# Kernel tuning notes

Hardware: AMD Instinct MI355X
Metric: run time of the kernel (lower is better)

Reference implementation:

```python
import jax, jax.numpy as jnp
import numpy as np

D = 768
H = 12
DH = D // H
PAIRS4 = [(0, 1), (0, 2), (0, 3), (1, 2), (1, 3), (2, 3)]
J6 = jnp.array([[0,0,0,0,0,1],[0,0,0,0,-1,0],[0,0,0,1,0,0],[0,0,1,0,0,0],[0,-1,0,0,0,0],[1,0,0,0,0,0]], dtype=jnp.float32)


def exterior(p1, p2):
    # p1,p2: (..., 4) -> normalized Plucker coords (..., 6)
    parts = [p1[..., i] * p2[..., j] - p1[..., j] * p2[..., i] for i, j in PAIRS4]
    L = jnp.stack(parts, axis=-1)
    n = jnp.clip(jnp.linalg.norm(L, axis=-1, keepdims=True), 1e-12)
    return L / n


def layernorm(x, g, b, eps=1e-5):
    m = jnp.mean(x, axis=-1, keepdims=True)
    v = jnp.var(x, axis=-1, keepdims=True)
    return (x - m) * jax.lax.rsqrt(v + eps) * g + b


def setup_inputs() -> dict:
    key = jax.random.key(0)
    ks = jax.random.split(key, 16)
    s = 0.02
    inp = {
        'x': jax.random.normal(ks[0], (1, 2048, D), dtype=jnp.float32),
        'ln1_g': jnp.ones((D,), jnp.float32), 'ln1_b': jnp.zeros((D,), jnp.float32),
        'qkv_w': jax.random.normal(ks[1], (D, 3 * D), jnp.float32) * s,
        'qkv_b': jnp.zeros((3 * D,), jnp.float32),
        'w1_write': jax.random.normal(ks[2], (D, 4 * H), jnp.float32) * s,
        'w2_write': jax.random.normal(ks[3], (D, 4 * H), jnp.float32) * s,
        'w1_read': jax.random.normal(ks[4], (D, 4 * H), jnp.float32) * s,
        'w2_read': jax.random.normal(ks[5], (D, 4 * H), jnp.float32) * s,
        'geo_v_w': jax.random.normal(ks[6], (D, D), jnp.float32) * s,
        'geo_v_b': jnp.zeros((D,), jnp.float32),
        'gate_w': jax.random.normal(ks[7], (D, H), jnp.float32) * s,
        'gate_b': jnp.zeros((H,), jnp.float32),
        'inc_scale': jnp.ones((H,), jnp.float32),
        'out_w': jax.random.normal(ks[8], (D, D), jnp.float32) * s,
        'out_b': jnp.zeros((D,), jnp.float32),
        'ln2_g': jnp.ones((D,), jnp.float32), 'ln2_b': jnp.zeros((D,), jnp.float32),
        'fc_w': jax.random.normal(ks[9], (D, 4 * D), jnp.float32) * s,
        'fc_b': jnp.zeros((4 * D,), jnp.float32),
        'proj_w': jax.random.normal(ks[10], (4 * D, D), jnp.float32) * s,
        'proj_b': jnp.zeros((D,), jnp.float32),
    }
    return inp


def dual_path_attention(x, qkv_w, qkv_b, w1_write, w2_write, w1_read, w2_read,
                        geo_v_w, geo_v_b, gate_w, gate_b, inc_scale, out_w, out_b):
    B, T, _ = x.shape
    scale = DH ** -0.5
    qkv = (x @ qkv_w + qkv_b).reshape(B, T, 3, H, DH)
    q = qkv[:, :, 0].transpose(0, 2, 1, 3)  # (B,H,T,dh)
    k = qkv[:, :, 1].transpose(0, 2, 1, 3)
    v = qkv[:, :, 2].transpose(0, 2, 1, 3)
    std_logits = jnp.einsum('bhtd,bhsd->bhts', q, k) * scale

    x_prev = jnp.concatenate([jnp.zeros((B, 1, x.shape[-1]), x.dtype), x[:, :-1]], axis=1)
    w1 = (x_prev @ w1_write).reshape(B, T, H, 4)
    w2 = (x @ w2_write).reshape(B, T, H, 4)
    write_lines = exterior(w1, w2)  # (B,T,H,6)
    r1 = (x @ w1_read).reshape(B, T, H, 4)
    r2 = (x @ w2_read).reshape(B, T, H, 4)
    read_lines = exterior(r1, r2)
    J_write = jnp.einsum('bthi,ij->bthj', write_lines, J6)
    geo_logits = jnp.einsum('bthp,bshp->bhts', read_lines, J_write)
    geo_logits = geo_logits * inc_scale[None, :, None, None]

    mask = jnp.triu(jnp.ones((T, T), dtype=bool), k=1)  # True above diagonal
    neg = jnp.finfo(x.dtype).min
    std_attn = jax.nn.softmax(jnp.where(mask, neg, std_logits), axis=-1)
    std_out = jnp.einsum('bhts,bhsd->bthd', std_attn, v).reshape(B, T, -1)
    geo_attn = jax.nn.softmax(jnp.where(mask, neg, geo_logits), axis=-1)
    geo_v = (x @ geo_v_w + geo_v_b).reshape(B, T, H, DH).transpose(0, 2, 1, 3)
    geo_out = jnp.einsum('bhts,bhsd->bthd', geo_attn, geo_v).reshape(B, T, -1)

    gate = jax.nn.sigmoid(x @ gate_w + gate_b).mean(axis=-1, keepdims=True)
    combined = (1 - gate) * std_out + gate * geo_out
    return combined @ out_w + out_b


def reference(x, ln1_g, ln1_b, qkv_w, qkv_b, w1_write, w2_write, w1_read, w2_read,
              geo_v_w, geo_v_b, gate_w, gate_b, inc_scale, out_w, out_b,
              ln2_g, ln2_b, fc_w, fc_b, proj_w, proj_b):
    h = x + dual_path_attention(layernorm(x, ln1_g, ln1_b), qkv_w, qkv_b,
                                w1_write, w2_write, w1_read, w2_read,
                                geo_v_w, geo_v_b, gate_w, gate_b, inc_scale,
                                out_w, out_b)
    m = layernorm(h, ln2_g, ln2_b)
    mlp = jax.nn.gelu(m @ fc_w + fc_b) @ proj_w + proj_b
    return h + mlp
```

## Files before the change

### kernel.cpp

```cpp
#include <hip/hip_runtime.h>
#include <hip/hip_bf16.h>
#include <math.h>

#define TT 2048
#define DD 768

typedef __bf16 bf16x8 __attribute__((ext_vector_type(8)));
typedef float f32x4 __attribute__((ext_vector_type(4)));

__device__ __forceinline__ void gload16(const void* g, void* l) {
    __builtin_amdgcn_global_load_lds(
        (const __attribute__((address_space(1))) unsigned int*)g,
        (__attribute__((address_space(3))) unsigned int*)l, 16, 0, 0);
}

__device__ __forceinline__ bf16x8 zero8() {
    bf16x8 v;
    #pragma unroll
    for (int j = 0; j < 8; ++j) v[j] = (__bf16)0.0f;
    return v;
}

__device__ __forceinline__ const __hip_bfloat16* opart_cptr(
    const __hip_bfloat16* pA, const __hip_bfloat16* pB, const __hip_bfloat16* pC, int slot)
{
    if (slot < 192) return pA + (size_t)slot * 8192;
    if (slot < 576) return pB + (size_t)(slot - 192) * 8192;
    return pC + (size_t)(slot - 576) * 8192;
}

__global__ __launch_bounds__(256) void ln_kernel(const float* __restrict__ in,
    const float* __restrict__ g, const float* __restrict__ b,
    __hip_bfloat16* __restrict__ out)
{
    const int t = blockIdx.x;
    const int tid = threadIdx.x;
    const float* row = in + (size_t)t * DD;
    float x0 = row[tid], x1 = row[tid + 256], x2 = row[tid + 512];
    float s = x0 + x1 + x2;
    float q = x0 * x0 + x1 * x1 + x2 * x2;
    #pragma unroll
    for (int m = 1; m < 64; m <<= 1) {
        s += __shfl_xor(s, m);
        q += __shfl_xor(q, m);
    }
    __shared__ float ssum[4], sqsum[4];
    const int w = tid >> 6;
    if ((tid & 63) == 0) { ssum[w] = s; sqsum[w] = q; }
    __syncthreads();
    s = ssum[0] + ssum[1] + ssum[2] + ssum[3];
    q = sqsum[0] + sqsum[1] + sqsum[2] + sqsum[3];
    const float mean = s * (1.0f / DD);
    const float var = q * (1.0f / DD) - mean * mean;
    const float rs = rsqrtf(var + 1e-5f);
    __hip_bfloat16* orow = out + (size_t)t * DD;
    orow[tid]       = __float2bfloat16((x0 - mean) * rs * g[tid]       + b[tid]);
    orow[tid + 256] = __float2bfloat16((x1 - mean) * rs * g[tid + 256] + b[tid + 256]);
    orow[tid + 512] = __float2bfloat16((x2 - mean) * rs * g[tid + 512] + b[tid + 512]);
}

__global__ __launch_bounds__(256) void castT_kernel(const float* __restrict__ in,
    __hip_bfloat16* __restrict__ out, int K, int N)
{
    __shared__ float t[32][33];
    const int n0 = blockIdx.x << 5, k0 = blockIdx.y << 5;
    const int tx = threadIdx.x & 31, ty = threadIdx.x >> 5;
    #pragma unroll
    for (int i = 0; i < 32; i += 8)
        t[ty + i][tx] = in[(size_t)(k0 + ty + i) * N + n0 + tx];
    __syncthreads();
    #pragma unroll
    for (int i = 0; i < 32; i += 8)
        out[(size_t)(n0 + ty + i) * K + k0 + tx] = __float2bfloat16(t[tx][ty + i]);
}

__global__ __launch_bounds__(256) void wcat_kernel(
    const float* __restrict__ w2w, const float* __restrict__ w1w,
    const float* __restrict__ w1r, const float* __restrict__ w2r,
    const float* __restrict__ gw, const float* __restrict__ qkv_b,
    const float* __restrict__ gvb, __hip_bfloat16* __restrict__ Wcat,
    float* __restrict__ bias3)
{
    const int bid = blockIdx.x;
    const int tid = threadIdx.x;
    if (bid >= 204) {
        const int idx = (bid - 204) * 256 + tid;
        float v = (idx < 2304) ? qkv_b[idx] : ((idx < 3072) ? gvb[idx - 2304] : 0.f);
        bias3[idx] = v;
        return;
    }
    const float* src; int col, stride;
    if (bid < 48)       { src = w2w; col = bid;       stride = 48; }
    else if (bid < 96)  { src = w1w; col = bid - 48;  stride = 48; }
    else if (bid < 144) { src = w1r; col = bid - 96;  stride = 48; }
    else if (bid < 192) { src = w2r; col = bid - 144; stride = 48; }
    else                { src = gw;  col = bid - 192; stride = 12; }
    #pragma unroll
    for (int i = 0; i < 3; ++i) {
        const int k = tid + (i << 8);
        Wcat[(size_t)bid * 768 + k] = __float2bfloat16(src[(size_t)k * stride + col]);
    }
}

__device__ __forceinline__ float gelu_f(float x) {
    float u = 0.7978845608028654f * (x + 0.044715f * x * x * x);
    return 0.5f * x * (1.0f + tanhf(u));
}

__global__ __launch_bounds__(256) void mgemm64_kernel(
    const __hip_bfloat16* __restrict__ A, const __hip_bfloat16* __restrict__ Bt,
    const float* __restrict__ bias, const float* __restrict__ resid,
    void* __restrict__ Cout, float* __restrict__ Pb0, float* __restrict__ Pb1,
    int M, int N, int K, int kz, int epi, int omode)
{
    __shared__ __hip_bfloat16 As[64 * 32];
    __shared__ __hip_bfloat16 Bs[128 * 32];
    const int tid = threadIdx.x;
    const int lane = tid & 63, w = tid >> 6;
    const int colBase = blockIdx.x << 7, rowBase = blockIdx.y << 6;
    const int z = blockIdx.z;
    const int Kc = K / kz, koff = z * Kc;

    const int lr = lane >> 2, pc = lane & 3;
    const int n = lane & 15, quad = lane >> 4;

    const int arow = (w << 4) + lr;
    const int ac = (pc ^ ((arow >> 1) & 3)) << 3;
    const int brow0 = (w << 5) + lr, brow1 = brow0 + 16;
    const int bc0 = (pc ^ ((brow0 >> 1) & 3)) << 3;
    const int bc1 = (pc ^ ((brow1 >> 1) & 3)) << 3;

    f32x4 acc[8];
    #pragma unroll
    for (int j = 0; j < 8; ++j) acc[j] = (f32x4){0.f, 0.f, 0.f, 0.f};

    const int arF = (w << 4) + n;
    const int aposF = (quad ^ ((arF >> 1) & 3)) << 3;

    for (int kk = koff; kk < koff + Kc; kk += 32) {
        __syncthreads();
        gload16(A  + (size_t)(rowBase + arow) * K + kk + ac,   &As[(w << 4) * 32]);
        gload16(Bt + (size_t)(colBase + brow0) * K + kk + bc0, &Bs[(w << 5) * 32]);
        gload16(Bt + (size_t)(colBase + brow1) * K + kk + bc1, &Bs[((w << 5) + 16) * 32]);
        __syncthreads();

        bf16x8 af = *(const bf16x8*)&As[arF * 32 + aposF];
        #pragma unroll
        for (int j = 0; j < 8; ++j) {
            const int rb = (j << 4) + n;
            bf16x8 bfj = *(const bf16x8*)&Bs[rb * 32 + ((quad ^ ((rb >> 1) & 3)) << 3)];
            acc[j] = __builtin_amdgcn_mfma_f32_16x16x32_bf16(af, bfj, acc[j], 0, 0, 0);
        }
    }

    if (kz == 1) {
        #pragma unroll
        for (int j = 0; j < 8; ++j) {
            const int col = colBase + (j << 4) + n;
            const float bj = bias ? bias[col] : 0.f;
            #pragma unroll
            for (int r = 0; r < 4; ++r) {
                const int row = rowBase + (w << 4) + (quad << 2) + r;
                float v = acc[j][r] + bj;
                if (epi == 1) v = gelu_f(v);
                else if (epi == 2) v += resid[(size_t)row * N + col];
                if (omode == 1) ((__hip_bfloat16*)Cout)[(size_t)row * N + col] = __float2bfloat16(v);
                else ((float*)Cout)[(size_t)row * N + col] = v;
            }
        }
    } else {
        float* P = (z == 0) ? Pb0 : Pb1;
        #pragma unroll
        for (int j = 0; j < 8; ++j) {
            const int col = colBase + (j << 4) + n;
            #pragma unroll
            for (int r = 0; r < 4; ++r) {
                const int row = rowBase + (w << 4) + (quad << 2) + r;
                P[(size_t)row * N + col] = acc[j][r];
            }
        }
    }
}

__global__ __launch_bounds__(256) void kred_kernel(
    const float* __restrict__ p0, const float* __restrict__ p1,
    const float* __restrict__ bias, const float* __restrict__ resid,
    float* __restrict__ out, int N)
{
    const int base = (blockIdx.x * 256 + threadIdx.x) << 2;
    float4 a = *(const float4*)&p0[base];
    float4 b = *(const float4*)&p1[base];
    float4 bi = *(const float4*)&bias[base % N];
    float4 rs = *(const float4*)&resid[base];
    float4 o;
    o.x = a.x + b.x + bi.x + rs.x;
    o.y = a.y + b.y + bi.y + rs.y;
    o.z = a.z + b.z + bi.z + rs.z;
    o.w = a.w + b.w + bi.w + rs.w;
    *(float4*)&out[base] = o;
}

__device__ __forceinline__ void exterior6(const float* a, const float* b, float* L) {
    L[0] = a[0] * b[1] - a[1] * b[0];
    L[1] = a[0] * b[2] - a[2] * b[0];
    L[2] = a[0] * b[3] - a[3] * b[0];
    L[3] = a[1] * b[2] - a[2] * b[1];
    L[4] = a[1] * b[3] - a[3] * b[1];
    L[5] = a[2] * b[3] - a[3] * b[2];
    float n = sqrtf(L[0]*L[0] + L[1]*L[1] + L[2]*L[2] + L[3]*L[3] + L[4]*L[4] + L[5]*L[5]);
    float inv = 1.f / fmaxf(n, 1e-12f);
    #pragma unroll
    for (int p = 0; p < 6; ++p) L[p] *= inv;
}

__global__ __launch_bounds__(64) void extgate_kernel(
    const __hip_bfloat16* __restrict__ Pall, const float* __restrict__ gb,
    __hip_bfloat16* __restrict__ rlb, __hip_bfloat16* __restrict__ jwb,
    float* __restrict__ gate)
{
    const int t = blockIdx.x;
    const int tid = threadIdx.x;
    const __hip_bfloat16* row = Pall + (size_t)t * 3328 + 3072;
    if (tid < 12) {
        const int h = tid;
        float a[4], b[4], L[6];
        #pragma unroll
        for (int i = 0; i < 4; ++i) {
            a[i] = (t > 0) ? __bfloat162float(row[-3328 + 48 + h * 4 + i]) : 0.f;
            b[i] = __bfloat162float(row[h * 4 + i]);
        }
        exterior6(a, b, L);
        __hip_bfloat16* jwp = jwb + (size_t)h * 16384 + t * 8;
        jwp[0] = __float2bfloat16( L[5]); jwp[1] = __float2bfloat16(-L[4]);
        jwp[2] = __float2bfloat16( L[3]); jwp[3] = __float2bfloat16( L[2]);
        jwp[4] = __float2bfloat16(-L[1]); jwp[5] = __float2bfloat16( L[0]);
        jwp[6] = __float2bfloat16(0.f);   jwp[7] = __float2bfloat16(0.f);
        #pragma unroll
        for (int i = 0; i < 4; ++i) {
            a[i] = __bfloat162float(row[96 + h * 4 + i]);
            b[i] = __bfloat162float(row[144 + h * 4 + i]);
        }
        exterior6(a, b, L);
        __hip_bfloat16* rlp = rlb + (size_t)h * 16384 + t * 8;
        #pragma unroll
        for (int p = 0; p < 6; ++p) rlp[p] = __float2bfloat16(L[p]);
        rlp[6] = __float2bfloat16(0.f); rlp[7] = __float2bfloat16(0.f);
    }
    if (tid == 32) {
        float g = 0.f;
        #pragma unroll
        for (int i = 0; i < 12; ++i)
            g += 1.f / (1.f + __expf(-(__bfloat162float(row[192 + i]) + gb[i])));
        gate[t] = g * (1.f / 12.f);
    }
}

__global__ __launch_bounds__(256) void vt_kernel(
    const __hip_bfloat16* __restrict__ qkvAll,
    __hip_bfloat16* __restrict__ VT, __hip_bfloat16* __restrict__ GVT)
{
    __shared__ __hip_bfloat16 tile[64][72];
    const int s0 = blockIdx.x << 6, h = blockIdx.y;
    const bool isGV = (blockIdx.z != 0);
    const __hip_bfloat16* src = qkvAll + (isGV ? 2304 : 1536) + h * 64;
    __hip_bfloat16* dst = (isGV ? GVT : VT) + (size_t)h * 131072;
    const int tid = threadIdx.x;
    const int r = tid >> 2, c = (tid & 3) << 3;
    *(bf16x8*)&tile[r][c]      = *(const bf16x8*)&src[(size_t)(s0 + r) * 3328 + c];
    *(bf16x8*)&tile[r][c + 32] = *(const bf16x8*)&src[(size_t)(s0 + r) * 3328 + c + 32];
    __syncthreads();
    __hip_bfloat16 tmp[8];
    #pragma unroll
    for (int j = 0; j < 8; ++j) tmp[j] = tile[c + j][r];
    *(bf16x8*)&dst[(size_t)r * 2048 + s0 + c] = *(const bf16x8*)tmp;
    #pragma unroll
    for (int j = 0; j < 8; ++j) tmp[j] = tile[c + 32 + j][r];
    *(bf16x8*)&dst[(size_t)r * 2048 + s0 + c + 32] = *(const bf16x8*)tmp;
}

__global__ __launch_bounds__(256) void mattn_kernel(
    const __hip_bfloat16* __restrict__ qkvAll, const __hip_bfloat16* __restrict__ VT,
    const __hip_bfloat16* __restrict__ GVT, const __hip_bfloat16* __restrict__ rlb,
    const __hip_bfloat16* __restrict__ jwb, const float* __restrict__ gate,
    const float* __restrict__ inc_scale, __hip_bfloat16* __restrict__ comb,
    __hip_bfloat16* __restrict__ OpA, __hip_bfloat16* __restrict__ OpB,
    __hip_bfloat16* __restrict__ OpC, float* __restrict__ stats)
{
    __shared__ __hip_bfloat16 Ks0[2048], Ks1[2048];
    __shared__ __hip_bfloat16 VTs0[2048], VTs1[2048];
    __shared__ __hip_bfloat16 GVTs0[2048], GVTs1[2048];
    __shared__ __hip_bfloat16 JWs[64][8];
    __shared__ __bf16 Ps[64][72];

    const int j = blockIdx.x;
    const int hh = blockIdx.y;
    int qt = 0, acc = 0, nc = 1;
    #pragma unroll 1
    for (;;) {
        nc = (qt + 9) / 9;
        if (j < acc + nc) break;
        acc += nc; ++qt;
    }
    const int c = j - acc;
    const int q0 = qt << 6;
    const int nk = qt + 1;
    const int ktb = c * nk / nc;
    const int kte = (c + 1) * nk / nc - 1;
    const int tid = threadIdx.x;
    const int w = tid >> 6, lane = tid & 63;
    const int n = lane & 15, quad = lane >> 4;

    const int qrow = q0 + (w << 4) + n;
    const size_t qb = (size_t)qrow * 3328 + hh * 64;
    bf16x8 af0 = *(const bf16x8*)&qkvAll[qb + (quad << 3)];
    bf16x8 af1 = *(const bf16x8*)&qkvAll[qb + 32 + (quad << 3)];
    bf16x8 rlA = zero8();
    if (quad == 0) rlA = *(const bf16x8*)&rlb[(size_t)hh * 16384 + (size_t)qrow * 8];
    const float isc = inc_scale[hh];
    const float mgc = fabsf(isc);
    const size_t vbase = (size_t)hh * 131072;

    const int sRow = tid >> 2, sc = tid & 3;
    const int sPos = ((sc ^ ((sRow >> 1) & 3)) << 3);
    const int sOff = sc << 3;

    f32x4 Os[4], Og[4];
    float m_s[4], lsp[4], lgp[4];
    #pragma unroll
    for (int r = 0; r < 4; ++r) {
        m_s[r] = -1e30f; lsp[r] = 0.f; lgp[r] = 0.f;
        Os[r] = (f32x4){0.f, 0.f, 0.f, 0.f};
        Og[r] = (f32x4){0.f, 0.f, 0.f, 0.f};
    }

    bf16x8 rK0, rK1, rV0, rV1, rG0, rG1, rJ = zero8();
    {
        const int k0 = ktb << 6;
        const size_t kb = (size_t)(k0 + sRow) * 3328 + 768 + hh * 64;
        const size_t vb = vbase + (size_t)sRow * 2048 + k0;
        rK0 = *(const bf16x8*)&qkvAll[kb + sOff];
        rK1 = *(const bf16x8*)&qkvAll[kb + sOff + 32];
        rV0 = *(const bf16x8*)&VT[vb + sOff];
        rV1 = *(const bf16x8*)&VT[vb + sOff + 32];
        rG0 = *(const bf16x8*)&GVT[vb + sOff];
        rG1 = *(const bf16x8*)&GVT[vb + sOff + 32];
        if (tid < 64) rJ = *(const bf16x8*)&jwb[(size_t)hh * 16384 + (size_t)(k0 + tid) * 8];
    }

    for (int kt = ktb; kt <= kte; ++kt) {
        const int k0 = kt << 6;
        __syncthreads();
        *(bf16x8*)&Ks0[sRow * 32 + sPos]  = rK0;
        *(bf16x8*)&Ks1[sRow * 32 + sPos]  = rK1;
        *(bf16x8*)&VTs0[sRow * 32 + sPos] = rV0;
        *(bf16x8*)&VTs1[sRow * 32 + sPos] = rV1;
        *(bf16x8*)&GVTs0[sRow * 32 + sPos] = rG0;
        *(bf16x8*)&GVTs1[sRow * 32 + sPos] = rG1;
        if (tid < 64) *(bf16x8*)&JWs[tid][0] = rJ;
        if (kt < kte) {
            const int k1 = (kt + 1) << 6;
            const size_t kb = (size_t)(k1 + sRow) * 3328 + 768 + hh * 64;
            const size_t vb = vbase + (size_t)sRow * 2048 + k1;
            rK0 = *(const bf16x8*)&qkvAll[kb + sOff];
            rK1 = *(const bf16x8*)&qkvAll[kb + sOff + 32];
            rV0 = *(const bf16x8*)&VT[vb + sOff];
            rV1 = *(const bf16x8*)&VT[vb + sOff + 32];
            rG0 = *(const bf16x8*)&GVT[vb + sOff];
            rG1 = *(const bf16x8*)&GVT[vb + sOff + 32];
            if (tid < 64) rJ = *(const bf16x8*)&jwb[(size_t)hh * 16384 + (size_t)(k1 + tid) * 8];
        }
        __syncthreads();

        f32x4 Ss[4], Sg[4];
        #pragma unroll
        for (int t = 0; t < 4; ++t) {
            Ss[t] = (f32x4){0.f, 0.f, 0.f, 0.f};
            Sg[t] = (f32x4){0.f, 0.f, 0.f, 0.f};
        }
        #pragma unroll
        for (int t = 0; t < 4; ++t) {
            const int krow = (t << 4) + n;
            const int kpos = ((quad ^ ((krow >> 1) & 3)) << 3);
            bf16x8 kb0 = *(const bf16x8*)&Ks0[krow * 32 + kpos];
            bf16x8 kb1 = *(const bf16x8*)&Ks1[krow * 32 + kpos];
            Ss[t] = __builtin_amdgcn_mfma_f32_16x16x32_bf16(af0, kb0, Ss[t], 0, 0, 0);
            Ss[t] = __builtin_amdgcn_mfma_f32_16x16x32_bf16(af1, kb1, Ss[t], 0, 0, 0);
            bf16x8 jb = zero8();
            if (quad == 0) jb = *(const bf16x8*)&JWs[krow][0];
            Sg[t] = __builtin_amdgcn_mfma_f32_16x16x32_bf16(rlA, jb, Sg[t], 0, 0, 0);
        }
        #pragma unroll
        for (int t = 0; t < 4; ++t) {
            #pragma unroll
            for (int r = 0; r < 4; ++r) { Ss[t][r] *= 0.125f; Sg[t][r] *= isc; }
        }
        if (kt == qt) {
            #pragma unroll
            for (int t = 0; t < 4; ++t) {
                const int sg = k0 + (t << 4) + n;
                #pragma unroll
                for (int r = 0; r < 4; ++r) {
                    const int qg = q0 + (w << 4) + (quad << 2) + r;
                    if (sg > qg) { Ss[t][r] = -1e30f; Sg[t][r] = -1e30f; }
                }
            }
        }

        #pragma unroll
        for (int r = 0; r < 4; ++r) {
            float mx = fmaxf(fmaxf(Ss[0][r], Ss[1][r]), fmaxf(Ss[2][r], Ss[3][r]));
            #pragma unroll
            for (int mk = 1; mk < 16; mk <<= 1) mx = fmaxf(mx, __shfl_xor(mx, mk));
            float mnew = fmaxf(m_s[r], mx);
            float alpha = __expf(m_s[r] - mnew);
            m_s[r] = mnew;
            float sm = 0.f;
            #pragma unroll
            for (int t = 0; t < 4; ++t) { Ss[t][r] = __expf(Ss[t][r] - mnew); sm += Ss[t][r]; }
            lsp[r] = lsp[r] * alpha + sm;
            #pragma unroll
            for (int t = 0; t < 4; ++t) Os[t][r] *= alpha;

            float smg = 0.f;
            #pragma unroll
            for (int t = 0; t < 4; ++t) { Sg[t][r] = __expf(Sg[t][r] - mgc); smg += Sg[t][r]; }
            lgp[r] += smg;
        }

        #pragma unroll
        for (int t = 0; t < 4; ++t) {
            #pragma unroll
            for (int r = 0; r < 4; ++r)
                Ps[(w << 4) + (quad << 2) + r][(t << 4) + n] = (__bf16)Ss[t][r];
        }
        asm volatile("s_waitcnt lgkmcnt(0)" ::: "memory");
        #pragma unroll
        for (int st = 0; st < 2; ++st) {
            bf16x8 ap = *(const bf16x8*)&Ps[(w << 4) + n][(st << 5) + (quad << 3)];
            const __hip_bfloat16* Vh = st ? VTs1 : VTs0;
            #pragma unroll
            for (int dt = 0; dt < 4; ++dt) {
                const int vrow = (dt << 4) + n;
                const int vpos = ((quad ^ ((vrow >> 1) & 3)) << 3);
                bf16x8 vb2 = *(const bf16x8*)&Vh[vrow * 32 + vpos];
                Os[dt] = __builtin_amdgcn_mfma_f32_16x16x32_bf16(ap, vb2, Os[dt], 0, 0, 0);
            }
        }
        asm volatile("s_waitcnt lgkmcnt(0)" ::: "memory");

        #pragma unroll
        for (int t = 0; t < 4; ++t) {
            #pragma unroll
            for (int r = 0; r < 4; ++r)
                Ps[(w << 4) + (quad << 2) + r][(t << 4) + n] = (__bf16)Sg[t][r];
        }
        asm volatile("s_waitcnt lgkmcnt(0)" ::: "memory");
        #pragma unroll
        for (int st = 0; st < 2; ++st) {
            bf16x8 gp = *(const bf16x8*)&Ps[(w << 4) + n][(st << 5) + (quad << 3)];
            const __hip_bfloat16* Gh = st ? GVTs1 : GVTs0;
            #pragma unroll
            for (int dt = 0; dt < 4; ++dt) {
                const int vrow = (dt << 4) + n;
                const int vpos = ((quad ^ ((vrow >> 1) & 3)) << 3);
                bf16x8 gb2 = *(const bf16x8*)&Gh[vrow * 32 + vpos];
                Og[dt] = __builtin_amdgcn_mfma_f32_16x16x32_bf16(gp, gb2, Og[dt], 0, 0, 0);
            }
        }
    }

    float l_s[4], l_g[4];
    #pragma unroll
    for (int r = 0; r < 4; ++r) {
        float ls = lsp[r], lg = lgp[r];
        #pragma unroll
        for (int mk = 1; mk < 16; mk <<= 1) {
            ls += __shfl_xor(ls, mk);
            lg += __shfl_xor(lg, mk);
        }
        l_s[r] = ls; l_g[r] = lg;
    }

    if (nc == 1) {
        #pragma unroll
        for (int r = 0; r < 4; ++r) {
            const int row = q0 + (w << 4) + (quad << 2) + r;
            const float g = gate[row];
            const float invs = (1.f - g) / l_s[r], invg = g / l_g[r];
            #pragma unroll
            for (int dt = 0; dt < 4; ++dt) {
                float val = Os[dt][r] * invs + Og[dt][r] * invg;
                comb[(size_t)row * DD + hh * 64 + (dt << 4) + n] = __float2bfloat16(val);
            }
        }
    } else {
        const int slot = hh * 74 + acc + c;
        __hip_bfloat16* op = (__hip_bfloat16*)opart_cptr(OpA, OpB, OpC, slot);
        float* st = stats + (size_t)slot * 256;
        #pragma unroll
        for (int r = 0; r < 4; ++r) {
            const int rloc = (w << 4) + (quad << 2) + r;
            #pragma unroll
            for (int dt = 0; dt < 4; ++dt) {
                const int col = (dt << 4) + n;
                op[rloc * 128 + col]      = __float2bfloat16(Os[dt][r]);
                op[rloc * 128 + 64 + col] = __float2bfloat16(Og[dt][r]);
            }
            if (n == 0) {
                st[rloc * 4 + 0] = m_s[r]; st[rloc * 4 + 1] = l_s[r];
                st[rloc * 4 + 2] = mgc;    st[rloc * 4 + 3] = l_g[r];
            }
        }
    }
}

__global__ __launch_bounds__(256) void acomb_kernel(
    const __hip_bfloat16* __restrict__ OpA, const __hip_bfloat16* __restrict__ OpB,
    const __hip_bfloat16* __restrict__ OpC, const float* __restrict__ stats,
    const float* __restrict__ gate, __hip_bfloat16* __restrict__ comb)
{
    const int qt = 9 + blockIdx.x;
    const int h = blockIdx.y;
    const int nc = (qt + 9) / 9;
    int acc = 0;
    #pragma unroll 1
    for (int q = 0; q < qt; ++q) acc += (q + 9) / 9;
    const int sb = h * 74 + acc;
    const int tid = threadIdx.x;
    const int rloc = tid >> 2;
    const int cseg = (tid & 3) << 4;
    const int row = (qt << 6) + rloc;
    float ms = -1e30f, mg = -1e30f;
    for (int c = 0; c < nc; ++c) {
        const float* st = stats + (size_t)(sb + c) * 256 + rloc * 4;
        ms = fmaxf(ms, st[0]);
        mg = fmaxf(mg, st[2]);
    }
    float wsc[4], wgc[4];
    float ls = 0.f, lg = 0.f;
    for (int c = 0; c < nc; ++c) {
        const float* st = stats + (size_t)(sb + c) * 256 + rloc * 4;
        wsc[c] = __expf(st[0] - ms); ls += st[1] * wsc[c];
        wgc[c] = __expf(st[2] - mg); lg += st[3] * wgc[c];
    }
    const float g = gate[row];
    const float fs = (1.f - g) / ls, fg = g / lg;
    #pragma unroll
    for (int cc = 0; cc < 16; ++cc) {
        const int col = cseg + cc;
        float os = 0.f, og = 0.f;
        for (int c = 0; c < nc; ++c) {
            const __hip_bfloat16* op = opart_cptr(OpA, OpB, OpC, sb + c) + rloc * 128;
            os += __bfloat162float(op[col]) * wsc[c];
            og += __bfloat162float(op[64 + col]) * wgc[c];
        }
        comb[(size_t)row * DD + h * 64 + col] = __float2bfloat16(os * fs + og * fg);
    }
}

extern "C" void kernel_launch(void* const* d_in, const int* in_sizes, int n_in,
                              void* d_out, int out_size, void* d_ws, size_t ws_size,
                              hipStream_t stream) {
    (void)in_sizes; (void)n_in; (void)out_size; (void)ws_size;
    const float* x      = (const float*)d_in[0];
    const float* ln1_g  = (const float*)d_in[1];
    const float* ln1_b  = (const float*)d_in[2];
    const float* qkv_w  = (const float*)d_in[3];
    const float* qkv_b  = (const float*)d_in[4];
    const float* w1w    = (const float*)d_in[5];
    const float* w2w    = (const float*)d_in[6];
    const float* w1r    = (const float*)d_in[7];
    const float* w2r    = (const float*)d_in[8];
    const float* gvw    = (const float*)d_in[9];
    const float* gvb    = (const float*)d_in[10];
    const float* gw     = (const float*)d_in[11];
    const float* gb     = (const float*)d_in[12];
    const float* isc    = (const float*)d_in[13];
    const float* ow     = (const float*)d_in[14];
    const float* ob     = (const float*)d_in[15];
    const float* ln2_g  = (const float*)d_in[16];
    const float* ln2_b  = (const float*)d_in[17];
    const float* fcw    = (const float*)d_in[18];
    const float* fcb    = (const float*)d_in[19];
    const float* pw     = (const float*)d_in[20];
    const float* pb     = (const float*)d_in[21];
    float* out = (float*)d_out;
    char* wsb  = (char*)d_ws;

    __hip_bfloat16* qkvAll = (__hip_bfloat16*)(wsb + 0);
    __hip_bfloat16* VTb    = (__hip_bfloat16*)(wsb + 13631488);
    __hip_bfloat16* GVTb   = (__hip_bfloat16*)(wsb + 16777216);
    __hip_bfloat16* rlb    = (__hip_bfloat16*)(wsb + 19922944);
    __hip_bfloat16* jwb    = (__hip_bfloat16*)(wsb + 20316160);
    float*          gate   = (float*)(wsb + 20709376);
    __hip_bfloat16* ln1    = (__hip_bfloat16*)(wsb + 20717568);
    __hip_bfloat16* comb   = (__hip_bfloat16*)(wsb + 23863296);
    float*          hbuf   = (float*)(wsb + 27009024);
    __hip_bfloat16* Bt     = (__hip_bfloat16*)(wsb + 33300480);
    float*          bias3  = (float*)(wsb + 38412288);
    __hip_bfloat16* owt    = (__hip_bfloat16*)(wsb + 38425600);

    __hip_bfloat16* OpA   = ln1;
    __hip_bfloat16* OpB   = (__hip_bfloat16*)hbuf;
    __hip_bfloat16* OpC   = Bt;
    float*          stats = (float*)owt;

    __hip_bfloat16* fcact  = qkvAll;
    __hip_bfloat16* pwt    = VTb;
    __hip_bfloat16* fcwt   = Bt;
    float* Ppart0 = (float*)(wsb + 20717568);
    float* Ppart1 = (float*)(wsb + 33300480);

    castT_kernel<<<dim3(72, 24), 256, 0, stream>>>(qkv_w, Bt, 768, 2304);
    castT_kernel<<<dim3(24, 24), 256, 0, stream>>>(gvw, Bt + (size_t)2304 * 768, 768, 768);
    wcat_kernel<<<217, 256, 0, stream>>>(w2w, w1w, w1r, w2r, gw, qkv_b, gvb,
                                         Bt + (size_t)3072 * 768, bias3);
    ln_kernel<<<TT, 256, 0, stream>>>(x, ln1_g, ln1_b, ln1);
    mgemm64_kernel<<<dim3(26, 32, 1), 256, 0, stream>>>(ln1, Bt, bias3, nullptr, qkvAll,
                                                        nullptr, nullptr, TT, 3328, 768, 1, 0, 1);
    extgate_kernel<<<TT, 64, 0, stream>>>(qkvAll, gb, rlb, jwb, gate);
    vt_kernel<<<dim3(32, 12, 2), 256, 0, stream>>>(qkvAll, VTb, GVTb);
    mattn_kernel<<<dim3(74, 12), 256, 0, stream>>>(qkvAll, VTb, GVTb, rlb, jwb, gate, isc,
                                                   comb, OpA, OpB, OpC, stats);
    acomb_kernel<<<dim3(23, 12), 256, 0, stream>>>(OpA, OpB, OpC, stats, gate, comb);
    castT_kernel<<<dim3(24, 24), 256, 0, stream>>>(ow, owt, 768, 768);
    mgemm64_kernel<<<dim3(6, 32, 1), 256, 0, stream>>>(comb, owt, ob, x, hbuf,
                                                       nullptr, nullptr, TT, 768, 768, 1, 2, 0);
    ln_kernel<<<TT, 256, 0, stream>>>(hbuf, ln2_g, ln2_b, ln1);
    castT_kernel<<<dim3(96, 24), 256, 0, stream>>>(fcw, fcwt, 768, 3072);
    mgemm64_kernel<<<dim3(24, 32, 1), 256, 0, stream>>>(ln1, fcwt, fcb, nullptr, fcact,
                                                        nullptr, nullptr, TT, 3072, 768, 1, 1, 1);
    castT_kernel<<<dim3(24, 96), 256, 0, stream>>>(pw, pwt, 3072, 768);
    mgemm64_kernel<<<dim3(6, 32, 2), 256, 0, stream>>>(fcact, pwt, pb, nullptr, nullptr,
                                                       Ppart0, Ppart1, TT, 768, 3072, 2, 0, 0);
    kred_kernel<<<1536, 256, 0, stream>>>(Ppart0, Ppart1, pb, hbuf, out, 768);
}
```

Measured before the change: 341.8 us.

## Load attention K/V tiles directly from global memory and merge weight-cast launches

The attention kernel no longer stages K, V, geo-V and JW tiles through swizzled shared memory with register prefetch and two barriers per key tile. Each wave now reads MFMA operands straight from global memory, and a separate Pg buffer lets the standard and geo probability tiles be written once and consumed in a single fused PV loop. This removes barriers and LDS traffic, but every wave now redundantly fetches the same K/V data, which relies on L1/L2 hits and exposes global-load latency. Separately, the six weight transpose/cast launches are merged into two prep_kernel launches to cut launch overhead.

```diff
diff --git a/kernel.cpp b/kernel.cpp
--- a/kernel.cpp
+++ b/kernel.cpp
@@ -59,46 +59,59 @@
     orow[tid + 512] = __float2bfloat16((x2 - mean) * rs * g[tid + 512] + b[tid + 512]);
 }
 
-__global__ __launch_bounds__(256) void castT_kernel(const float* __restrict__ in,
-    __hip_bfloat16* __restrict__ out, int K, int N)
-{
-    __shared__ float t[32][33];
-    const int n0 = blockIdx.x << 5, k0 = blockIdx.y << 5;
-    const int tx = threadIdx.x & 31, ty = threadIdx.x >> 5;
+__device__ __forceinline__ void castT_body(const float* __restrict__ in,
+    __hip_bfloat16* __restrict__ out, int K, int N, int bx, int by, int tid,
+    float (*tt)[33])
+{
+    const int n0 = bx << 5, k0 = by << 5;
+    const int tx = tid & 31, ty = tid >> 5;
     #pragma unroll
     for (int i = 0; i < 32; i += 8)
-        t[ty + i][tx] = in[(size_t)(k0 + ty + i) * N + n0 + tx];
+        tt[ty + i][tx] = in[(size_t)(k0 + ty + i) * N + n0 + tx];
     __syncthreads();
     #pragma unroll
     for (int i = 0; i < 32; i += 8)
-        out[(size_t)(n0 + ty + i) * K + k0 + tx] = __float2bfloat16(t[tx][ty + i]);
-}
-
-__global__ __launch_bounds__(256) void wcat_kernel(
+        out[(size_t)(n0 + ty + i) * K + k0 + tx] = __float2bfloat16(tt[tx][ty + i]);
+}
+
+__global__ __launch_bounds__(256) void prep_kernel(
+    const float* __restrict__ w0, const float* __restrict__ w1, const float* __restrict__ w2,
     const float* __restrict__ w2w, const float* __restrict__ w1w,
     const float* __restrict__ w1r, const float* __restrict__ w2r,
     const float* __restrict__ gw, const float* __restrict__ qkv_b,
-    const float* __restrict__ gvb, __hip_bfloat16* __restrict__ Wcat,
-    float* __restrict__ bias3)
-{
+    const float* __restrict__ gvb,
+    __hip_bfloat16* __restrict__ o0, __hip_bfloat16* __restrict__ o1,
+    __hip_bfloat16* __restrict__ o2,
+    __hip_bfloat16* __restrict__ Wcat, float* __restrict__ bias3, int mode)
+{
+    __shared__ float tt[32][33];
     const int bid = blockIdx.x;
     const int tid = threadIdx.x;
-    if (bid >= 204) {
-        const int idx = (bid - 204) * 256 + tid;
-        float v = (idx < 2304) ? qkv_b[idx] : ((idx < 3072) ? gvb[idx - 2304] : 0.f);
-        bias3[idx] = v;
-        return;
-    }
-    const float* src; int col, stride;
-    if (bid < 48)       { src = w2w; col = bid;       stride = 48; }
-    else if (bid < 96)  { src = w1w; col = bid - 48;  stride = 48; }
-    else if (bid < 144) { src = w1r; col = bid - 96;  stride = 48; }
-    else if (bid < 192) { src = w2r; col = bid - 144; stride = 48; }
-    else                { src = gw;  col = bid - 192; stride = 12; }
-    #pragma unroll
-    for (int i = 0; i < 3; ++i) {
-        const int k = tid + (i << 8);
-        Wcat[(size_t)bid * 768 + k] = __float2bfloat16(src[(size_t)k * stride + col]);
+    if (mode == 0) {
+        if (bid < 1728)      { castT_body(w0, o0, 768, 2304, bid % 72, bid / 72, tid, tt); return; }
+        else if (bid < 2304) { int b = bid - 1728; castT_body(w1, o1, 768, 768, b % 24, b / 24, tid, tt); return; }
+        const int wb = bid - 2304;
+        if (wb >= 204) {
+            const int idx = (wb - 204) * 256 + tid;
+            float v = (idx < 2304) ? qkv_b[idx] : ((idx < 3072) ? gvb[idx - 2304] : 0.f);
+            bias3[idx] = v;
+            return;
+        }
+        const float* src; int col, stride;
+        if (wb < 48)       { src = w2w; col = wb;       stride = 48; }
+        else if (wb < 96)  { src = w1w; col = wb - 48;  stride = 48; }
+        else if (wb < 144) { src = w1r; col = wb - 96;  stride = 48; }
+        else if (wb < 192) { src = w2r; col = wb - 144; stride = 48; }
+        else               { src = gw;  col = wb - 192; stride = 12; }
+        #pragma unroll
+        for (int i = 0; i < 3; ++i) {
+            const int k = tid + (i << 8);
+            Wcat[(size_t)wb * 768 + k] = __float2bfloat16(src[(size_t)k * stride + col]);
+        }
+    } else {
+        if (bid < 576)       { castT_body(w0, o0, 768, 768, bid % 24, bid / 24, tid, tt); }
+        else if (bid < 2880) { int b = bid - 576;  castT_body(w1, o1, 768, 3072, b % 96, b / 96, tid, tt); }
+        else                 { int b = bid - 2880; castT_body(w2, o2, 3072, 768, b % 24, b / 24, tid, tt); }
     }
 }
 
@@ -286,11 +299,8 @@
     __hip_bfloat16* __restrict__ OpA, __hip_bfloat16* __restrict__ OpB,
     __hip_bfloat16* __restrict__ OpC, float* __restrict__ stats)
 {
-    __shared__ __hip_bfloat16 Ks0[2048], Ks1[2048];
-    __shared__ __hip_bfloat16 VTs0[2048], VTs1[2048];
-    __shared__ __hip_bfloat16 GVTs0[2048], GVTs1[2048];
-    __shared__ __hip_bfloat16 JWs[64][8];
     __shared__ __bf16 Ps[64][72];
+    __shared__ __bf16 Pg[64][72];
 
     const int j = blockIdx.x;
     const int hh = blockIdx.y;
@@ -319,10 +329,7 @@
     const float isc = inc_scale[hh];
     const float mgc = fabsf(isc);
     const size_t vbase = (size_t)hh * 131072;
-
-    const int sRow = tid >> 2, sc = tid & 3;
-    const int sPos = ((sc ^ ((sRow >> 1) & 3)) << 3);
-    const int sOff = sc << 3;
+    const size_t jwbase = (size_t)hh * 16384;
 
     f32x4 Os[4], Og[4];
     float m_s[4], lsp[4], lgp[4];
@@ -333,43 +340,8 @@
         Og[r] = (f32x4){0.f, 0.f, 0.f, 0.f};
     }
 
-    bf16x8 rK0, rK1, rV0, rV1, rG0, rG1, rJ = zero8();
-    {
-        const int k0 = ktb << 6;
-        const size_t kb = (size_t)(k0 + sRow) * 3328 + 768 + hh * 64;
-        const size_t vb = vbase + (size_t)sRow * 2048 + k0;
-        rK0 = *(const bf16x8*)&qkvAll[kb + sOff];
-        rK1 = *(const bf16x8*)&qkvAll[kb + sOff + 32];
-        rV0 = *(const bf16x8*)&VT[vb + sOff];
-        rV1 = *(const bf16x8*)&VT[vb + sOff + 32];
-        rG0 = *(const bf16x8*)&GVT[vb + sOff];
-        rG1 = *(const bf16x8*)&GVT[vb + sOff + 32];
-        if (tid < 64) rJ = *(const bf16x8*)&jwb[(size_t)hh * 16384 + (size_t)(k0 + tid) * 8];
-    }
-
     for (int kt = ktb; kt <= kte; ++kt) {
         const int k0 = kt << 6;
-        __syncthreads();
-        *(bf16x8*)&Ks0[sRow * 32 + sPos]  = rK0;
-        *(bf16x8*)&Ks1[sRow * 32 + sPos]  = rK1;
-        *(bf16x8*)&VTs0[sRow * 32 + sPos] = rV0;
-        *(bf16x8*)&VTs1[sRow * 32 + sPos] = rV1;
-        *(bf16x8*)&GVTs0[sRow * 32 + sPos] = rG0;
-        *(bf16x8*)&GVTs1[sRow * 32 + sPos] = rG1;
-        if (tid < 64) *(bf16x8*)&JWs[tid][0] = rJ;
-        if (kt < kte) {
-            const int k1 = (kt + 1) << 6;
-            const size_t kb = (size_t)(k1 + sRow) * 3328 + 768 + hh * 64;
-            const size_t vb = vbase + (size_t)sRow * 2048 + k1;
-            rK0 = *(const bf16x8*)&qkvAll[kb + sOff];
-            rK1 = *(const bf16x8*)&qkvAll[kb + sOff + 32];
-            rV0 = *(const bf16x8*)&VT[vb + sOff];
-            rV1 = *(const bf16x8*)&VT[vb + sOff + 32];
-            rG0 = *(const bf16x8*)&GVT[vb + sOff];
-            rG1 = *(const bf16x8*)&GVT[vb + sOff + 32];
-            if (tid < 64) rJ = *(const bf16x8*)&jwb[(size_t)hh * 16384 + (size_t)(k1 + tid) * 8];
-        }
-        __syncthreads();
 
         f32x4 Ss[4], Sg[4];
         #pragma unroll
@@ -379,14 +351,13 @@
         }
         #pragma unroll
         for (int t = 0; t < 4; ++t) {
-            const int krow = (t << 4) + n;
-            const int kpos = ((quad ^ ((krow >> 1) & 3)) << 3);
-            bf16x8 kb0 = *(const bf16x8*)&Ks0[krow * 32 + kpos];
-            bf16x8 kb1 = *(const bf16x8*)&Ks1[krow * 32 + kpos];
+            const int krow = k0 + (t << 4) + n;
+            const size_t kb = (size_t)krow * 3328 + 768 + hh * 64 + (quad << 3);
+            bf16x8 kb0 = *(const bf16x8*)&qkvAll[kb];
+            bf16x8 kb1 = *(const bf16x8*)&qkvAll[kb + 32];
+            bf16x8 jb  = *(const bf16x8*)&jwb[jwbase + (size_t)krow * 8];
             Ss[t] = __builtin_amdgcn_mfma_f32_16x16x32_bf16(af0, kb0, Ss[t], 0, 0, 0);
             Ss[t] = __builtin_amdgcn_mfma_f32_16x16x32_bf16(af1, kb1, Ss[t], 0, 0, 0);
-            bf16x8 jb = zero8();
-            if (quad == 0) jb = *(const bf16x8*)&JWs[krow][0];
             Sg[t] = __builtin_amdgcn_mfma_f32_16x16x32_bf16(rlA, jb, Sg[t], 0, 0, 0);
         }
         #pragma unroll
@@ -430,40 +401,24 @@
         #pragma unroll
         for (int t = 0; t < 4; ++t) {
             #pragma unroll
-            for (int r = 0; r < 4; ++r)
+            for (int r = 0; r < 4; ++r) {
                 Ps[(w << 4) + (quad << 2) + r][(t << 4) + n] = (__bf16)Ss[t][r];
+                Pg[(w << 4) + (quad << 2) + r][(t << 4) + n] = (__bf16)Sg[t][r];
+            }
         }
         asm volatile("s_waitcnt lgkmcnt(0)" ::: "memory");
+
         #pragma unroll
         for (int st = 0; st < 2; ++st) {
             bf16x8 ap = *(const bf16x8*)&Ps[(w << 4) + n][(st << 5) + (quad << 3)];
-            const __hip_bfloat16* Vh = st ? VTs1 : VTs0;
+            bf16x8 gp = *(const bf16x8*)&Pg[(w << 4) + n][(st << 5) + (quad << 3)];
             #pragma unroll
             for (int dt = 0; dt < 4; ++dt) {
                 const int vrow = (dt << 4) + n;
-                const int vpos = ((quad ^ ((vrow >> 1) & 3)) << 3);
-                bf16x8 vb2 = *(const bf16x8*)&Vh[vrow * 32 + vpos];
+                const size_t vb = vbase + (size_t)vrow * 2048 + k0 + (st << 5) + (quad << 3);
+                bf16x8 vb2 = *(const bf16x8*)&VT[vb];
+                bf16x8 gb2 = *(const bf16x8*)&GVT[vb];
                 Os[dt] = __builtin_amdgcn_mfma_f32_16x16x32_bf16(ap, vb2, Os[dt], 0, 0, 0);
-            }
-        }
-        asm volatile("s_waitcnt lgkmcnt(0)" ::: "memory");
-
-        #pragma unroll
-        for (int t = 0; t < 4; ++t) {
-            #pragma unroll
-            for (int r = 0; r < 4; ++r)
-                Ps[(w << 4) + (quad << 2) + r][(t << 4) + n] = (__bf16)Sg[t][r];
-        }
-        asm volatile("s_waitcnt lgkmcnt(0)" ::: "memory");
-        #pragma unroll
-        for (int st = 0; st < 2; ++st) {
-            bf16x8 gp = *(const bf16x8*)&Ps[(w << 4) + n][(st << 5) + (quad << 3)];
-            const __hip_bfloat16* Gh = st ? GVTs1 : GVTs0;
-            #pragma unroll
-            for (int dt = 0; dt < 4; ++dt) {
-                const int vrow = (dt << 4) + n;
-                const int vpos = ((quad ^ ((vrow >> 1) & 3)) << 3);
-                bf16x8 gb2 = *(const bf16x8*)&Gh[vrow * 32 + vpos];
                 Og[dt] = __builtin_amdgcn_mfma_f32_16x16x32_bf16(gp, gb2, Og[dt], 0, 0, 0);
             }
         }
@@ -611,10 +566,10 @@
     float* Ppart0 = (float*)(wsb + 20717568);
     float* Ppart1 = (float*)(wsb + 33300480);
 
-    castT_kernel<<<dim3(72, 24), 256, 0, stream>>>(qkv_w, Bt, 768, 2304);
-    castT_kernel<<<dim3(24, 24), 256, 0, stream>>>(gvw, Bt + (size_t)2304 * 768, 768, 768);
-    wcat_kernel<<<217, 256, 0, stream>>>(w2w, w1w, w1r, w2r, gw, qkv_b, gvb,
-                                         Bt + (size_t)3072 * 768, bias3);
+    prep_kernel<<<2521, 256, 0, stream>>>(qkv_w, gvw, nullptr,
+                                          w2w, w1w, w1r, w2r, gw, qkv_b, gvb,
+                                          Bt, Bt + (size_t)2304 * 768, nullptr,
+                                          Bt + (size_t)3072 * 768, bias3, 0);
     ln_kernel<<<TT, 256, 0, stream>>>(x, ln1_g, ln1_b, ln1);
     mgemm64_kernel<<<dim3(26, 32, 1), 256, 0, stream>>>(ln1, Bt, bias3, nullptr, qkvAll,
                                                         nullptr, nullptr, TT, 3328, 768, 1, 0, 1);
@@ -623,14 +578,15 @@
     mattn_kernel<<<dim3(74, 12), 256, 0, stream>>>(qkvAll, VTb, GVTb, rlb, jwb, gate, isc,
                                                    comb, OpA, OpB, OpC, stats);
     acomb_kernel<<<dim3(23, 12), 256, 0, stream>>>(OpA, OpB, OpC, stats, gate, comb);
-    castT_kernel<<<dim3(24, 24), 256, 0, stream>>>(ow, owt, 768, 768);
+    prep_kernel<<<5184, 256, 0, stream>>>(ow, fcw, pw,
+                                          nullptr, nullptr, nullptr, nullptr,
+                                          nullptr, nullptr, nullptr,
+                                          owt, fcwt, pwt, nullptr, nullptr, 1);
     mgemm64_kernel<<<dim3(6, 32, 1), 256, 0, stream>>>(comb, owt, ob, x, hbuf,
                                                        nullptr, nullptr, TT, 768, 768, 1, 2, 0);
     ln_kernel<<<TT, 256, 0, stream>>>(hbuf, ln2_g, ln2_b, ln1);
-    castT_kernel<<<dim3(96, 24), 256, 0, stream>>>(fcw, fcwt, 768, 3072);
     mgemm64_kernel<<<dim3(24, 32, 1), 256, 0, stream>>>(ln1, fcwt, fcb, nullptr, fcact,
                                                         nullptr, nullptr, TT, 3072, 768, 1, 1, 1);
-    castT_kernel<<<dim3(24, 96), 256, 0, stream>>>(pw, pwt, 3072, 768);
     mgemm64_kernel<<<dim3(6, 32, 2), 256, 0, stream>>>(fcact, pwt, pb, nullptr, nullptr,
                                                        Ppart0, Ppart1, TT, 768, 3072, 2, 0, 0);
     kred_kernel<<<1536, 256, 0, stream>>>(Ppart0, Ppart1, pb, hbuf, out, 768);
```

After: 390.2 us. +14.2%, slower.
